# Kernel optimization log

Hardware: AMD Instinct MI355X
Metric: run time of the kernel (lower is better)

## Reference

```python
import jax, jax.numpy as jnp
import numpy as np

B, CIN, T, H, W = 2, 256, 16, 16, 8
FF, COUT, NHEADS = 512, 256, 8
TEMP = 16.0
BN_EPS = 1e-5


def setup_inputs() -> dict:
    key = jax.random.key(0)
    ks = jax.random.split(key, 6)
    s_in = 1.0 / np.sqrt(CIN)
    s_ff = 1.0 / np.sqrt(FF)
    return {
        "x": jax.random.normal(ks[0], (B, CIN, T, H, W), jnp.float32),
        "WK": jax.random.uniform(ks[1], (FF, CIN), jnp.float32, -s_in, s_in),
        "WQ": jax.random.uniform(ks[2], (FF, CIN), jnp.float32, -s_in, s_in),
        "WV": jax.random.uniform(ks[3], (FF, CIN), jnp.float32, -s_in, s_in),
        "Wo": jax.random.uniform(ks[4], (COUT, FF), jnp.float32, -s_ff, s_ff),
        "bo": jax.random.uniform(ks[5], (COUT,), jnp.float32, -s_ff, s_ff),
        "gamma": jnp.ones((COUT,), jnp.float32),
        "beta": jnp.zeros((COUT,), jnp.float32),
    }


def reference(x, WK, WQ, WV, Wo, bo, gamma, beta):
    N = T * H * W
    xf = x.reshape(B, CIN, N)  # 1x1 conv3d == channel matmul
    dh = FF // NHEADS
    K = jnp.einsum("fc,bcn->bfn", WK, xf).reshape(B, NHEADS, dh, N)
    Q = jnp.einsum("fc,bcn->bfn", WQ, xf).reshape(B, NHEADS, dh, N)
    V = jnp.einsum("fc,bcn->bfn", WV, xf).reshape(B, NHEADS, dh, N)
    # KQ[b,h,i,j] = K_i . Q_j  (i = key token, j = query token, as in torch)
    KQ = jnp.einsum("bhdi,bhdj->bhij", K, Q) / TEMP
    # block-causal mask: token time index t = token_idx // (H*W); tril -> allow i >= j
    t_idx = jnp.arange(N) // (H * W)
    allow = t_idx[:, None] >= t_idx[None, :]  # (N, N)
    KQ = jnp.where(allow[None, None], KQ, -jnp.inf)
    attn = jax.nn.softmax(KQ, axis=3)  # softmax over j (last dim), as in torch
    # out[b,h,d,i] = sum_j V[b,h,d,j] * attn[b,h,i,j]
    Vo = jnp.einsum("bhdj,bhij->bhdi", V, attn).reshape(B, FF, N)
    y = jnp.einsum("of,bfn->bon", Wo, Vo) + bo[None, :, None]
    y = jax.nn.relu(y).reshape(B, COUT, T, H, W)
    out = x + y  # skip: out_dim == in_dim
    # BatchNorm3d (training-mode batch stats, biased var)
    mean = out.mean(axis=(0, 2, 3, 4), keepdims=True)
    var = out.var(axis=(0, 2, 3, 4), keepdims=True)
    norm = (out - mean) * jax.lax.rsqrt(var + BN_EPS)
    return norm * gamma[None, :, None, None, None] + beta[None, :, None, None, None]
```

## Files before the change

### kernel.cpp

```cpp
#include <hip/hip_runtime.h>
#include <math.h>

#define BB_   2
#define CIN_  256
#define NTOK_ 2048
#define FF_   512
#define COUT_ 256
#define NH_   8
#define DH_   64
#define HW_   128
#define BNEPS_ 1e-5f
#define SCALE_LOG2_ 0.09016844005556021f

typedef __attribute__((ext_vector_type(8))) short short8;
typedef __attribute__((ext_vector_type(4))) float f32x4;

__device__ inline unsigned short f2bf(float f) {
  union { float f; unsigned u; } v; v.f = f;
  unsigned r = (v.u + 0x7FFF + ((v.u >> 16) & 1)) >> 16;
  return (unsigned short)r;
}

__device__ __forceinline__ void dma16(const unsigned short* g, unsigned short* l) {
  __builtin_amdgcn_global_load_lds(
      (const __attribute__((address_space(1))) void*)g,
      (__attribute__((address_space(3))) void*)l, 16, 0, 0);
}

__global__ __launch_bounds__(256) void prep_kernel(
    const float* __restrict__ x, const float* __restrict__ WK,
    const float* __restrict__ WQ, const float* __restrict__ WV,
    const float* __restrict__ Wo, unsigned short* __restrict__ xT,
    unsigned short* __restrict__ Wkb, unsigned short* __restrict__ Wqb,
    unsigned short* __restrict__ Wvb, unsigned short* __restrict__ Wob) {
  __shared__ float T[64 * 65];
  const int tid = threadIdx.x;
  const int bid = blockIdx.x;
  if (bid < 256) {
    const int b = bid >> 7;
    const int rem = bid & 127;
    const int n0 = (rem >> 2) * 64;
    const int c0 = (rem & 3) * 64;
#pragma unroll
    for (int p = 0; p < 4; ++p) {
      const int idx = tid + 256 * p;
      const int row = idx >> 4, col = (idx & 15) * 4;
      const float4 v =
          *(const float4*)(x + (size_t)(b * CIN_ + c0 + row) * NTOK_ + n0 + col);
      T[row * 65 + col + 0] = v.x; T[row * 65 + col + 1] = v.y;
      T[row * 65 + col + 2] = v.z; T[row * 65 + col + 3] = v.w;
    }
    __syncthreads();
#pragma unroll
    for (int p = 0; p < 2; ++p) {
      const int idx = tid + 256 * p;
      const int nl = idx >> 3, c8 = (idx & 7) * 8;
      unsigned short u[8];
#pragma unroll
      for (int i = 0; i < 8; ++i) u[i] = f2bf(T[(c8 + i) * 65 + nl]);
      *(uint4*)(xT + ((size_t)(b * NTOK_ + n0 + nl)) * CIN_ + c0 + c8) =
          *(uint4*)u;
    }
  } else {
    const int t = bid - 256;
    const int which = t >> 5, blk = t & 31;
    const float* src = which == 0 ? WK : which == 1 ? WQ : which == 2 ? WV : Wo;
    unsigned short* dst = which == 0 ? Wkb : which == 1 ? Wqb : which == 2 ? Wvb : Wob;
    const int base = blk * 4096 + tid * 16;
#pragma unroll
    for (int p = 0; p < 4; ++p) {
      const float4 v = *(const float4*)(src + base + p * 4);
      ushort4 u;
      u.x = f2bf(v.x); u.y = f2bf(v.y); u.z = f2bf(v.z); u.w = f2bf(v.w);
      *(ushort4*)(dst + base + p * 4) = u;
    }
  }
}

__global__ __launch_bounds__(256, 3) void qkv_kernel(
    const unsigned short* __restrict__ xT, const unsigned short* __restrict__ Wkb,
    const unsigned short* __restrict__ Wqb, const unsigned short* __restrict__ Wvb,
    unsigned short* __restrict__ Kb, unsigned short* __restrict__ Qb,
    unsigned short* __restrict__ Vt) {
  __shared__ unsigned short Wsh[128 * 72];
  __shared__ unsigned short Xsh[64 * 72];
  const int tid = threadIdx.x;
  const int lane = tid & 63, w = tid >> 6;
  const int lx = lane & 15, q = lane >> 4;
  const int wm = w >> 1, wn = w & 1;
  const int n0 = blockIdx.x * 64;
  const int f0 = blockIdx.y * 128;
  const int b = blockIdx.z / 3, which = blockIdx.z % 3;
  const unsigned short* Wb = which == 0 ? Wkb : which == 1 ? Wqb : Wvb;

  const int srow = tid >> 3;
  const int soff = (tid & 7) * 8;
  const unsigned short* Wg = Wb + (size_t)(f0 + srow) * CIN_ + soff;
  const unsigned short* Xg = xT + ((size_t)(b * NTOK_ + n0 + srow)) * CIN_ + soff;

  uint4 wr[4], xr[2];
#pragma unroll
  for (int r = 0; r < 4; ++r) wr[r] = *(const uint4*)(Wg + (size_t)(32 * r) * CIN_);
#pragma unroll
  for (int r = 0; r < 2; ++r) xr[r] = *(const uint4*)(Xg + (size_t)(32 * r) * CIN_);

  f32x4 acc[4][2];
#pragma unroll
  for (int i = 0; i < 4; ++i)
#pragma unroll
    for (int j = 0; j < 2; ++j) acc[i][j] = (f32x4){0.f, 0.f, 0.f, 0.f};

  for (int kk = 0; kk < 4; ++kk) {
    __syncthreads();
#pragma unroll
    for (int r = 0; r < 4; ++r) *(uint4*)(Wsh + (srow + 32 * r) * 72 + soff) = wr[r];
#pragma unroll
    for (int r = 0; r < 2; ++r) *(uint4*)(Xsh + (srow + 32 * r) * 72 + soff) = xr[r];
    if (kk < 3) {
      const int c0 = (kk + 1) * 64;
#pragma unroll
      for (int r = 0; r < 4; ++r) wr[r] = *(const uint4*)(Wg + (size_t)(32 * r) * CIN_ + c0);
#pragma unroll
      for (int r = 0; r < 2; ++r) xr[r] = *(const uint4*)(Xg + (size_t)(32 * r) * CIN_ + c0);
    }
    __syncthreads();
    short8 xF[2][2];
#pragma unroll
    for (int i = 0; i < 2; ++i) {
      xF[i][0] = *(const short8*)(Xsh + (32 * wn + 16 * i + lx) * 72 + q * 8);
      xF[i][1] = *(const short8*)(Xsh + (32 * wn + 16 * i + lx) * 72 + 32 + q * 8);
    }
    if (which < 2) {
#pragma unroll
      for (int i = 0; i < 4; ++i) {
        const short8 w0 = *(const short8*)(Wsh + (64 * wm + 16 * i + lx) * 72 + q * 8);
        const short8 w1 = *(const short8*)(Wsh + (64 * wm + 16 * i + lx) * 72 + 32 + q * 8);
#pragma unroll
        for (int j = 0; j < 2; ++j) {
          acc[i][j] = __builtin_amdgcn_mfma_f32_16x16x32_bf16(w0, xF[j][0], acc[i][j], 0, 0, 0);
          acc[i][j] = __builtin_amdgcn_mfma_f32_16x16x32_bf16(w1, xF[j][1], acc[i][j], 0, 0, 0);
        }
      }
    } else {
#pragma unroll
      for (int jf = 0; jf < 4; ++jf) {
        const short8 w0 = *(const short8*)(Wsh + (64 * wm + 16 * jf + lx) * 72 + q * 8);
        const short8 w1 = *(const short8*)(Wsh + (64 * wm + 16 * jf + lx) * 72 + 32 + q * 8);
#pragma unroll
        for (int i = 0; i < 2; ++i) {
          acc[jf][i] = __builtin_amdgcn_mfma_f32_16x16x32_bf16(xF[i][0], w0, acc[jf][i], 0, 0, 0);
          acc[jf][i] = __builtin_amdgcn_mfma_f32_16x16x32_bf16(xF[i][1], w1, acc[jf][i], 0, 0, 0);
        }
      }
    }
  }

  const int h = (f0 >> 6) + wm;
  if (which < 2) {
    unsigned short* Y = (which == 0 ? Kb : Qb);
    const float sc = (which == 0) ? SCALE_LOG2_ : 1.0f;
#pragma unroll
    for (int i = 0; i < 4; ++i)
#pragma unroll
      for (int j = 0; j < 2; ++j) {
        const int n = n0 + 32 * wn + 16 * j + lx;
        const int d0 = 16 * i + 4 * q;
        ushort4 u;
        u.x = f2bf(acc[i][j][0] * sc); u.y = f2bf(acc[i][j][1] * sc);
        u.z = f2bf(acc[i][j][2] * sc); u.w = f2bf(acc[i][j][3] * sc);
        *(ushort4*)(Y + ((size_t)((b * NH_ + h) * NTOK_ + n)) * DH_ + d0) = u;
      }
  } else {
#pragma unroll
    for (int jf = 0; jf < 4; ++jf)
#pragma unroll
      for (int i = 0; i < 2; ++i) {
        const int d = 16 * jf + lx;
        const int n = n0 + 32 * wn + 16 * i + 4 * q;
        ushort4 u;
        u.x = f2bf(acc[jf][i][0]); u.y = f2bf(acc[jf][i][1]);
        u.z = f2bf(acc[jf][i][2]); u.w = f2bf(acc[jf][i][3]);
        *(ushort4*)(Vt + ((size_t)((b * NH_ + h) * DH_ + d)) * NTOK_ + n) = u;
      }
  }
}

__global__ __launch_bounds__(256, 2) void attn_kernel(
    const unsigned short* __restrict__ Kb, const unsigned short* __restrict__ Qb,
    const unsigned short* __restrict__ Vt, unsigned short* __restrict__ Ob) {
  __shared__ __align__(16) unsigned short Qbuf[2][8192];
  __shared__ __align__(16) unsigned short Vbuf[2][8192];
  __shared__ __align__(16) unsigned short Psh[4 * 16 * 72];

  const int tid = threadIdx.x;
  const int lane = tid & 63;
  const int w = tid >> 6;
  const int lx = lane & 15;
  const int q = lane >> 4;

  const int bid = blockIdx.x;
  const int u = bid >> 4;
  const int iblk = (u < 16) ? (31 - u) : (u - 16);
  const int bh = bid & 15;
  const int h = bh & 7, b = bh >> 3;
  const int i0 = iblk * 64;
  const int njt = (iblk >> 1) + 1;

  const size_t bhs = (size_t)b * NH_ + h;
  const unsigned short* Kg = Kb + bhs * (size_t)NTOK_ * DH_ + (size_t)i0 * DH_;
  const unsigned short* Qg = Qb + bhs * (size_t)NTOK_ * DH_;
  const unsigned short* Vg = Vt + bhs * (size_t)DH_ * NTOK_;

  auto stage = [&](int buf, int j0) {
#pragma unroll
    for (int cc = 0; cc < 4; ++cc) {
      const int chunk = 4 * w + cc;
      {
        const int row = chunk * 8 + (lane >> 3);
        const int grp = (lane & 7) ^ (row & 7);
        dma16(Qg + (size_t)(j0 + row) * DH_ + grp * 8, &Qbuf[buf][chunk * 512]);
      }
      {
        const int row = chunk * 4 + (lane >> 4);
        const int grp = (lane & 15) ^ (row & 7);
        dma16(Vg + (size_t)row * NTOK_ + j0 + grp * 8, &Vbuf[buf][chunk * 512]);
      }
    }
  };

  const short8 aK0 = *(const short8*)(Kg + (16 * w + lx) * DH_ + q * 8);
  const short8 aK1 = *(const short8*)(Kg + (16 * w + lx) * DH_ + 32 + q * 8);

  unsigned short* Pw = Psh + w * 16 * 72;

  f32x4 o[4];
#pragma unroll
  for (int s = 0; s < 4; ++s) o[s] = (f32x4){0.f, 0.f, 0.f, 0.f};
  float rsum[4] = {0.f, 0.f, 0.f, 0.f};

  const int fr0 = ((q ^ (lx & 7)) << 3);
  const int fr1 = (((4 + q) ^ (lx & 7)) << 3);
  int frv[4];
#pragma unroll
  for (int kk = 0; kk < 4; ++kk) frv[kk] = (((4 * kk + q) ^ (lx & 7)) << 3);

  stage(0, 0);
  __syncthreads();

  int cur = 0;
  for (int jt = 0; jt < njt; ++jt) {
    if (jt + 1 < njt) stage(cur ^ 1, (jt + 1) * 128);

    const unsigned short* Qs = Qbuf[cur];
    const unsigned short* Vs = Vbuf[cur];

    f32x4 sa[8];
#pragma unroll
    for (int s = 0; s < 8; ++s) {
      const int row = 16 * s + lx;
      const short8 b0 = *(const short8*)(Qs + row * 64 + fr0);
      const short8 b1 = *(const short8*)(Qs + row * 64 + fr1);
      sa[s] = (f32x4){0.f, 0.f, 0.f, 0.f};
      sa[s] = __builtin_amdgcn_mfma_f32_16x16x32_bf16(aK0, b0, sa[s], 0, 0, 0);
      sa[s] = __builtin_amdgcn_mfma_f32_16x16x32_bf16(aK1, b1, sa[s], 0, 0, 0);
    }

#pragma unroll
    for (int half = 0; half < 2; ++half) {
#pragma unroll
      for (int s2 = 0; s2 < 4; ++s2)
#pragma unroll
        for (int r = 0; r < 4; ++r) {
          const float p = __builtin_amdgcn_exp2f(sa[4 * half + s2][r]);
          rsum[r] += p;
          Pw[(q * 4 + r) * 72 + 16 * s2 + lx] =
              (unsigned short)(__builtin_bit_cast(unsigned, p) >> 16);
        }
      asm volatile("s_waitcnt lgkmcnt(0)" ::: "memory");

      const short8 pb0 = *(const short8*)(Pw + lx * 72 + q * 8);
      const short8 pb1 = *(const short8*)(Pw + lx * 72 + 32 + q * 8);
#pragma unroll
      for (int s = 0; s < 4; ++s) {
        const int row = 16 * s + lx;
        const short8 va0 = *(const short8*)(Vs + row * 128 + frv[2 * half + 0]);
        const short8 va1 = *(const short8*)(Vs + row * 128 + frv[2 * half + 1]);
        o[s] = __builtin_amdgcn_mfma_f32_16x16x32_bf16(va0, pb0, o[s], 0, 0, 0);
        o[s] = __builtin_amdgcn_mfma_f32_16x16x32_bf16(va1, pb1, o[s], 0, 0, 0);
      }
      asm volatile("" ::: "memory");
    }

    __syncthreads();
    cur ^= 1;
  }

#pragma unroll
  for (int r = 0; r < 4; ++r) {
#pragma unroll
    for (int off = 1; off < 16; off <<= 1) rsum[r] += __shfl_xor(rsum[r], off);
  }
  const int gsrc = ((lx >> 2) << 4);
  const float u0 = __shfl(rsum[0], gsrc);
  const float u1 = __shfl(rsum[1], gsrc);
  const float u2 = __shfl(rsum[2], gsrc);
  const float u3 = __shfl(rsum[3], gsrc);
  const float lsel = (lx & 2) ? ((lx & 1) ? u3 : u2) : ((lx & 1) ? u1 : u0);
  const float invl = 1.0f / lsel;
  const int n = i0 + 16 * w + lx;
#pragma unroll
  for (int s = 0; s < 4; ++s) {
    ushort4 uo;
    uo.x = f2bf(o[s][0] * invl); uo.y = f2bf(o[s][1] * invl);
    uo.z = f2bf(o[s][2] * invl); uo.w = f2bf(o[s][3] * invl);
    *(ushort4*)(Ob + ((size_t)(b * NTOK_ + n)) * FF_ + h * 64 + 16 * s + 4 * q) = uo;
  }
}

__global__ __launch_bounds__(256) void proj_kernel(
    const unsigned short* __restrict__ Ob, const unsigned short* __restrict__ Wob,
    const float* __restrict__ bo, const float* __restrict__ x,
    float* __restrict__ pre) {
  __shared__ unsigned short Osh[64 * 72];
  __shared__ unsigned short Wsh[64 * 72];
  const int tid = threadIdx.x;
  const int lane = tid & 63, w = tid >> 6;
  const int lx = lane & 15, q = lane >> 4;
  const int wn = w & 1, wo = w >> 1;
  const int n0 = blockIdx.x * 64;
  const int o0 = blockIdx.y * 64;
  const int b = blockIdx.z;

  const int srow = tid >> 3;
  const int soff = (tid & 7) * 8;
  const unsigned short* Og = Ob + ((size_t)(b * NTOK_ + n0 + srow)) * FF_ + soff;
  const unsigned short* Wg = Wob + (size_t)(o0 + srow) * FF_ + soff;

  uint4 orr[2], wrr[2];
#pragma unroll
  for (int r = 0; r < 2; ++r) {
    orr[r] = *(const uint4*)(Og + (size_t)(32 * r) * FF_);
    wrr[r] = *(const uint4*)(Wg + (size_t)(32 * r) * FF_);
  }

  f32x4 acc[2][2];
#pragma unroll
  for (int i = 0; i < 2; ++i)
#pragma unroll
    for (int j = 0; j < 2; ++j) acc[i][j] = (f32x4){0.f, 0.f, 0.f, 0.f};

  for (int kk = 0; kk < 8; ++kk) {
    __syncthreads();
#pragma unroll
    for (int r = 0; r < 2; ++r) {
      *(uint4*)(Osh + (srow + 32 * r) * 72 + soff) = orr[r];
      *(uint4*)(Wsh + (srow + 32 * r) * 72 + soff) = wrr[r];
    }
    if (kk < 7) {
      const int c0 = (kk + 1) * 64;
#pragma unroll
      for (int r = 0; r < 2; ++r) {
        orr[r] = *(const uint4*)(Og + (size_t)(32 * r) * FF_ + c0);
        wrr[r] = *(const uint4*)(Wg + (size_t)(32 * r) * FF_ + c0);
      }
    }
    __syncthreads();
    short8 aF[2][2], bF[2][2];
#pragma unroll
    for (int i = 0; i < 2; ++i) {
      aF[i][0] = *(const short8*)(Osh + (32 * wn + 16 * i + lx) * 72 + q * 8);
      aF[i][1] = *(const short8*)(Osh + (32 * wn + 16 * i + lx) * 72 + 32 + q * 8);
      bF[i][0] = *(const short8*)(Wsh + (32 * wo + 16 * i + lx) * 72 + q * 8);
      bF[i][1] = *(const short8*)(Wsh + (32 * wo + 16 * i + lx) * 72 + 32 + q * 8);
    }
#pragma unroll
    for (int i = 0; i < 2; ++i)
#pragma unroll
      for (int j = 0; j < 2; ++j) {
        acc[i][j] = __builtin_amdgcn_mfma_f32_16x16x32_bf16(aF[i][0], bF[j][0], acc[i][j], 0, 0, 0);
        acc[i][j] = __builtin_amdgcn_mfma_f32_16x16x32_bf16(aF[i][1], bF[j][1], acc[i][j], 0, 0, 0);
      }
  }

#pragma unroll
  for (int j = 0; j < 2; ++j) {
    const int o = o0 + 32 * wo + 16 * j + lx;
    const float bias = bo[o];
#pragma unroll
    for (int i = 0; i < 2; ++i) {
      const int n = n0 + 32 * wn + 16 * i + 4 * q;
      const float4 xv = *(const float4*)(x + ((size_t)(b * CIN_ + o)) * NTOK_ + n);
      float4 v;
      v.x = fmaxf(acc[i][j][0] + bias, 0.f) + xv.x;
      v.y = fmaxf(acc[i][j][1] + bias, 0.f) + xv.y;
      v.z = fmaxf(acc[i][j][2] + bias, 0.f) + xv.z;
      v.w = fmaxf(acc[i][j][3] + bias, 0.f) + xv.w;
      *(float4*)(pre + ((size_t)(b * COUT_ + o)) * NTOK_ + n) = v;
    }
  }
}

__global__ __launch_bounds__(256) void bn_kernel(
    float* __restrict__ out, const float* __restrict__ gamma,
    const float* __restrict__ beta) {
  __shared__ float red[8];
  const int c = blockIdx.x;
  const int tid = threadIdx.x;
  const int lane = tid & 63, w = tid >> 6;

  float4 v[2][2];
  float s = 0.f, s2 = 0.f;
#pragma unroll
  for (int b = 0; b < BB_; ++b) {
    float* base = out + ((size_t)(b * COUT_ + c)) * NTOK_;
#pragma unroll
    for (int p = 0; p < 2; ++p) {
      const float4 t = *(const float4*)(base + 4 * tid + p * 1024);
      v[b][p] = t;
      s += t.x + t.y + t.z + t.w;
      s2 += t.x * t.x + t.y * t.y + t.z * t.z + t.w * t.w;
    }
  }
#pragma unroll
  for (int off = 32; off >= 1; off >>= 1) {
    s += __shfl_xor(s, off);
    s2 += __shfl_xor(s2, off);
  }
  if (lane == 0) { red[w] = s; red[4 + w] = s2; }
  __syncthreads();
  const float S = red[0] + red[1] + red[2] + red[3];
  const float S2 = red[4] + red[5] + red[6] + red[7];
  const float inv = 1.0f / (float)(BB_ * NTOK_);
  const float mean = S * inv;
  const float var = S2 * inv - mean * mean;
  const float sc = rsqrtf(var + BNEPS_) * gamma[c];
  const float bt = beta[c];
#pragma unroll
  for (int b = 0; b < BB_; ++b) {
    float* base = out + ((size_t)(b * COUT_ + c)) * NTOK_;
#pragma unroll
    for (int p = 0; p < 2; ++p) {
      float4 t = v[b][p];
      t.x = (t.x - mean) * sc + bt;
      t.y = (t.y - mean) * sc + bt;
      t.z = (t.z - mean) * sc + bt;
      t.w = (t.w - mean) * sc + bt;
      *(float4*)(base + 4 * tid + p * 1024) = t;
    }
  }
}

extern "C" void kernel_launch(void* const* d_in, const int* in_sizes, int n_in,
                              void* d_out, int out_size, void* d_ws, size_t ws_size,
                              hipStream_t stream) {
  (void)in_sizes; (void)n_in; (void)out_size; (void)ws_size;
  const float* x = (const float*)d_in[0];
  const float* WK = (const float*)d_in[1];
  const float* WQ = (const float*)d_in[2];
  const float* WV = (const float*)d_in[3];
  const float* Wo = (const float*)d_in[4];
  const float* bo = (const float*)d_in[5];
  const float* gamma = (const float*)d_in[6];
  const float* beta = (const float*)d_in[7];

  char* ws = (char*)d_ws;
  unsigned short* xT  = (unsigned short*)(ws);
  unsigned short* Wkb = (unsigned short*)(ws + 2097152);
  unsigned short* Wqb = (unsigned short*)(ws + 2359296);
  unsigned short* Wvb = (unsigned short*)(ws + 2621440);
  unsigned short* Wob = (unsigned short*)(ws + 2883584);
  unsigned short* Kb  = (unsigned short*)(ws + 3145728);
  unsigned short* Qb  = (unsigned short*)(ws + 7340032);
  unsigned short* Vt  = (unsigned short*)(ws + 11534336);
  unsigned short* Ob  = (unsigned short*)(ws + 15728640);
  float* out = (float*)d_out;

  prep_kernel<<<384, 256, 0, stream>>>(x, WK, WQ, WV, Wo, xT, Wkb, Wqb, Wvb, Wob);
  qkv_kernel<<<dim3(32, 4, 6), 256, 0, stream>>>(xT, Wkb, Wqb, Wvb, Kb, Qb, Vt);
  attn_kernel<<<dim3(512, 1, 1), 256, 0, stream>>>(Kb, Qb, Vt, Ob);
  proj_kernel<<<dim3(32, 4, 2), 256, 0, stream>>>(Ob, Wob, bo, x, out);
  bn_kernel<<<256, 256, 0, stream>>>(out, gamma, beta);
}
```

Before: 142.0 us.

## Keep softmax probabilities in registers by transposing QK MFMA operands

Swaps the operand order of the score MFMA so each lane's accumulator holds the layout needed as the B operand of a 16x16x16 bf16 MFMA for the PV product. The LDS round trip for P (store, waitcnt, reload) is removed, and the row-sum reduction shrinks to two cross-lane shuffles. In exchange, PV now issues twice as many smaller 16x16x16 MFMAs, with narrower 8-byte V reads from LDS.

```diff
diff --git a/kernel.cpp b/kernel.cpp
--- a/kernel.cpp
+++ b/kernel.cpp
@@ -13,7 +13,14 @@
 #define SCALE_LOG2_ 0.09016844005556021f
 
 typedef __attribute__((ext_vector_type(8))) short short8;
+typedef __attribute__((ext_vector_type(4))) short bfx4;
 typedef __attribute__((ext_vector_type(4))) float f32x4;
+
+#if __has_builtin(__builtin_amdgcn_mfma_f32_16x16x16_bf16)
+#define MFMA16(a, b, c) __builtin_amdgcn_mfma_f32_16x16x16_bf16(a, b, c, 0, 0, 0)
+#else
+#define MFMA16(a, b, c) __builtin_amdgcn_mfma_f32_16x16x16bf16_1k(a, b, c, 0, 0, 0)
+#endif
 
 __device__ inline unsigned short f2bf(float f) {
   union { float f; unsigned u; } v; v.f = f;
@@ -190,13 +197,12 @@
     const unsigned short* __restrict__ Vt, unsigned short* __restrict__ Ob) {
   __shared__ __align__(16) unsigned short Qbuf[2][8192];
   __shared__ __align__(16) unsigned short Vbuf[2][8192];
-  __shared__ __align__(16) unsigned short Psh[4 * 16 * 72];
 
   const int tid = threadIdx.x;
   const int lane = tid & 63;
   const int w = tid >> 6;
   const int lx = lane & 15;
-  const int q = lane >> 4;
+  const int g = lane >> 4;
 
   const int bid = blockIdx.x;
   const int u = bid >> 4;
@@ -228,21 +234,16 @@
     }
   };
 
-  const short8 aK0 = *(const short8*)(Kg + (16 * w + lx) * DH_ + q * 8);
-  const short8 aK1 = *(const short8*)(Kg + (16 * w + lx) * DH_ + 32 + q * 8);
-
-  unsigned short* Pw = Psh + w * 16 * 72;
+  const short8 aK0 = *(const short8*)(Kg + (16 * w + lx) * DH_ + g * 8);
+  const short8 aK1 = *(const short8*)(Kg + (16 * w + lx) * DH_ + 32 + g * 8);
 
   f32x4 o[4];
 #pragma unroll
-  for (int s = 0; s < 4; ++s) o[s] = (f32x4){0.f, 0.f, 0.f, 0.f};
-  float rsum[4] = {0.f, 0.f, 0.f, 0.f};
-
-  const int fr0 = ((q ^ (lx & 7)) << 3);
-  const int fr1 = (((4 + q) ^ (lx & 7)) << 3);
-  int frv[4];
-#pragma unroll
-  for (int kk = 0; kk < 4; ++kk) frv[kk] = (((4 * kk + q) ^ (lx & 7)) << 3);
+  for (int t = 0; t < 4; ++t) o[t] = (f32x4){0.f, 0.f, 0.f, 0.f};
+  float rs = 0.f;
+
+  const int fr0 = ((g ^ (lx & 7)) << 3);
+  const int fr1 = (((4 + g) ^ (lx & 7)) << 3);
 
   stage(0, 0);
   __syncthreads();
@@ -258,62 +259,50 @@
 #pragma unroll
     for (int s = 0; s < 8; ++s) {
       const int row = 16 * s + lx;
-      const short8 b0 = *(const short8*)(Qs + row * 64 + fr0);
-      const short8 b1 = *(const short8*)(Qs + row * 64 + fr1);
+      const short8 a0 = *(const short8*)(Qs + row * 64 + fr0);
+      const short8 a1 = *(const short8*)(Qs + row * 64 + fr1);
       sa[s] = (f32x4){0.f, 0.f, 0.f, 0.f};
-      sa[s] = __builtin_amdgcn_mfma_f32_16x16x32_bf16(aK0, b0, sa[s], 0, 0, 0);
-      sa[s] = __builtin_amdgcn_mfma_f32_16x16x32_bf16(aK1, b1, sa[s], 0, 0, 0);
-    }
-
-#pragma unroll
-    for (int half = 0; half < 2; ++half) {
-#pragma unroll
-      for (int s2 = 0; s2 < 4; ++s2)
-#pragma unroll
-        for (int r = 0; r < 4; ++r) {
-          const float p = __builtin_amdgcn_exp2f(sa[4 * half + s2][r]);
-          rsum[r] += p;
-          Pw[(q * 4 + r) * 72 + 16 * s2 + lx] =
-              (unsigned short)(__builtin_bit_cast(unsigned, p) >> 16);
-        }
-      asm volatile("s_waitcnt lgkmcnt(0)" ::: "memory");
-
-      const short8 pb0 = *(const short8*)(Pw + lx * 72 + q * 8);
-      const short8 pb1 = *(const short8*)(Pw + lx * 72 + 32 + q * 8);
-#pragma unroll
-      for (int s = 0; s < 4; ++s) {
-        const int row = 16 * s + lx;
-        const short8 va0 = *(const short8*)(Vs + row * 128 + frv[2 * half + 0]);
-        const short8 va1 = *(const short8*)(Vs + row * 128 + frv[2 * half + 1]);
-        o[s] = __builtin_amdgcn_mfma_f32_16x16x32_bf16(va0, pb0, o[s], 0, 0, 0);
-        o[s] = __builtin_amdgcn_mfma_f32_16x16x32_bf16(va1, pb1, o[s], 0, 0, 0);
-      }
-      asm volatile("" ::: "memory");
+      sa[s] = __builtin_amdgcn_mfma_f32_16x16x32_bf16(a0, aK0, sa[s], 0, 0, 0);
+      sa[s] = __builtin_amdgcn_mfma_f32_16x16x32_bf16(a1, aK1, sa[s], 0, 0, 0);
+    }
+
+#pragma unroll
+    for (int s = 0; s < 8; ++s) {
+      const float p0 = __builtin_amdgcn_exp2f(sa[s][0]);
+      const float p1 = __builtin_amdgcn_exp2f(sa[s][1]);
+      const float p2 = __builtin_amdgcn_exp2f(sa[s][2]);
+      const float p3 = __builtin_amdgcn_exp2f(sa[s][3]);
+      rs += (p0 + p1) + (p2 + p3);
+      union { unsigned u[2]; bfx4 v; } pk;
+      pk.u[0] = (__builtin_bit_cast(unsigned, p0) >> 16) |
+                (__builtin_bit_cast(unsigned, p1) & 0xFFFF0000u);
+      pk.u[1] = (__builtin_bit_cast(unsigned, p2) >> 16) |
+                (__builtin_bit_cast(unsigned, p3) & 0xFFFF0000u);
+      const int jgrp = 2 * s + (g >> 1);
+      const int joff = (g & 1) << 2;
+#pragma unroll
+      for (int t = 0; t < 4; ++t) {
+        const int row = 16 * t + lx;
+        const bfx4 va = *(const bfx4*)(Vs + row * 128 +
+                                       ((jgrp ^ (row & 7)) << 3) + joff);
+        o[t] = MFMA16(va, pk.v, o[t]);
+      }
     }
 
     __syncthreads();
     cur ^= 1;
   }
 
-#pragma unroll
-  for (int r = 0; r < 4; ++r) {
-#pragma unroll
-    for (int off = 1; off < 16; off <<= 1) rsum[r] += __shfl_xor(rsum[r], off);
-  }
-  const int gsrc = ((lx >> 2) << 4);
-  const float u0 = __shfl(rsum[0], gsrc);
-  const float u1 = __shfl(rsum[1], gsrc);
-  const float u2 = __shfl(rsum[2], gsrc);
-  const float u3 = __shfl(rsum[3], gsrc);
-  const float lsel = (lx & 2) ? ((lx & 1) ? u3 : u2) : ((lx & 1) ? u1 : u0);
-  const float invl = 1.0f / lsel;
+  rs += __shfl_xor(rs, 16);
+  rs += __shfl_xor(rs, 32);
+  const float invl = 1.0f / rs;
   const int n = i0 + 16 * w + lx;
 #pragma unroll
-  for (int s = 0; s < 4; ++s) {
+  for (int t = 0; t < 4; ++t) {
     ushort4 uo;
-    uo.x = f2bf(o[s][0] * invl); uo.y = f2bf(o[s][1] * invl);
-    uo.z = f2bf(o[s][2] * invl); uo.w = f2bf(o[s][3] * invl);
-    *(ushort4*)(Ob + ((size_t)(b * NTOK_ + n)) * FF_ + h * 64 + 16 * s + 4 * q) = uo;
+    uo.x = f2bf(o[t][0] * invl); uo.y = f2bf(o[t][1] * invl);
+    uo.z = f2bf(o[t][2] * invl); uo.w = f2bf(o[t][3] * invl);
+    *(ushort4*)(Ob + ((size_t)(b * NTOK_ + n)) * FF_ + h * 64 + 16 * t + 4 * g) = uo;
   }
 }
 
```

Result: no change. 139.9 us (-1.5%).
